# Kernel tuning notes

Hardware: AMD Instinct MI355X
Metric: run time of the kernel (lower is better)

Reference implementation:

```python
import jax, jax.numpy as jnp
import numpy as np

N_NODES = 50000
N_EDGES = 800000
IN_F = 128
HID = 64
HEADS = 4
N_CLASSES = 256
NEG_SLOPE = 0.2


def _gat_layer(h, W, al, ar, b, src, dst, act):
    """One DGL-style GATConv. h:[N,Din], W:[Din,H*F], al/ar:[H,F], b:[H*F].
    Returns [N,H,F]."""
    N = h.shape[0]
    H, F = al.shape
    z = (h @ W).reshape(N, H, F)                       # projected feats
    el = jnp.einsum('nhf,hf->nh', z, al)               # [N,H] src score part
    er = jnp.einsum('nhf,hf->nh', z, ar)               # [N,H] dst score part
    e = jax.nn.leaky_relu(el[src] + er[dst], negative_slope=NEG_SLOPE)  # [E,H]
    # segment softmax over incoming edges of each destination node
    emax = jax.ops.segment_max(e, dst, num_segments=N)                  # [N,H]
    ex = jnp.exp(e - emax[dst])                                         # [E,H]
    den = jax.ops.segment_sum(ex, dst, num_segments=N)                  # [N,H]
    alpha = ex / jnp.maximum(den[dst], 1e-9)                            # [E,H]
    msg = z[src] * alpha[:, :, None]                                    # [E,H,F]
    out = jax.ops.segment_sum(msg, dst, num_segments=N)                 # [N,H,F]
    out = out + b.reshape(1, H, F)
    return act(out) if act is not None else out


def setup_inputs() -> dict:
    key = jax.random.key(0)
    ks = jax.random.split(key, 16)
    feat = jax.random.normal(ks[0], (N_NODES, IN_F), dtype=jnp.float32)
    src = jax.random.randint(ks[1], (N_EDGES,), 0, N_NODES, dtype=jnp.int32)
    dst = jax.random.randint(ks[2], (N_EDGES,), 0, N_NODES, dtype=jnp.int32)

    def glorot(k, shape):
        fan = shape[0] + shape[-1]
        return jax.random.normal(k, shape, dtype=jnp.float32) * np.sqrt(2.0 / fan)

    # layer 0: IN_F -> HEADS*HID
    W0 = glorot(ks[3], (IN_F, HEADS * HID))
    al0 = glorot(ks[4], (HEADS, HID))
    ar0 = glorot(ks[5], (HEADS, HID))
    b0 = jnp.zeros((HEADS * HID,), dtype=jnp.float32)
    # layer 1: HEADS*HID -> HEADS*HID
    W1 = glorot(ks[6], (HEADS * HID, HEADS * HID))
    al1 = glorot(ks[7], (HEADS, HID))
    ar1 = glorot(ks[8], (HEADS, HID))
    b1 = jnp.zeros((HEADS * HID,), dtype=jnp.float32)
    # final layer: HEADS*HID -> HEADS*N_CLASSES
    W2 = glorot(ks[9], (HEADS * HID, HEADS * N_CLASSES))
    al2 = glorot(ks[10], (HEADS, N_CLASSES))
    ar2 = glorot(ks[11], (HEADS, N_CLASSES))
    b2 = jnp.zeros((HEADS * N_CLASSES,), dtype=jnp.float32)
    return {"feat": feat,
            "W0": W0, "al0": al0, "ar0": ar0, "b0": b0,
            "W1": W1, "al1": al1, "ar1": ar1, "b1": b1,
            "W2": W2, "al2": al2, "ar2": ar2, "b2": b2,
            "src": src, "dst": dst}


def reference(feat, W0, al0, ar0, b0, W1, al1, ar1, b1, W2, al2, ar2, b2, src, dst):
    elu = jax.nn.elu
    h = _gat_layer(feat, W0, al0, ar0, b0, src, dst, elu).reshape(N_NODES, -1)
    h = _gat_layer(h, W1, al1, ar1, b1, src, dst, elu).reshape(N_NODES, -1)
    logits = _gat_layer(h, W2, al2, ar2, b2, src, dst, None).mean(axis=1)  # [N, C]
    return logits
```

## Files before the change

kernel.cpp:

```cpp
#include <hip/hip_runtime.h>
#include <hip/hip_bf16.h>


#define NN 50000
#define NE 800000
#define NH_HEADS 4

typedef __attribute__((ext_vector_type(8))) short short8;
typedef __attribute__((ext_vector_type(8))) _Float16 half8;
typedef __attribute__((ext_vector_type(4))) _Float16 half4;
typedef __attribute__((ext_vector_type(4))) float floatx4;

__device__ inline float bf2f(short s) {
    union { unsigned u; float f; } v; v.u = ((unsigned)(unsigned short)s) << 16;
    return v.f;
}
__device__ inline short f2bf_rne(float x) {
    union { float f; unsigned u; } v; v.f = x;
    unsigned r = v.u + 0x7fff + ((v.u >> 16) & 1);
    return (short)(r >> 16);
}
__device__ inline void split1(float x, short& h, short& l) {
    union { float f; unsigned u; } v; v.f = x;
    h = (short)(v.u >> 16);
    union { float f; unsigned u; } rv; rv.f = v.f - bf2f(h);
    l = (short)(rv.u >> 16);
}

__device__ inline void load_lds16(const void* g, void* l) {
    __builtin_amdgcn_global_load_lds(
        (const __attribute__((address_space(1))) void*)g,
        (__attribute__((address_space(3))) void*)l, 16, 0, 0);
}


__global__ void hist_kernel(const int* __restrict__ dst, int* __restrict__ deg, int E) {
    int e = blockIdx.x * 256 + threadIdx.x;
    if (e < E) atomicAdd(&deg[dst[e]], 1);
}

__global__ void scan_block_kernel(const int* __restrict__ deg, int* __restrict__ offs,
                                  int* __restrict__ bsums, int n) {
    __shared__ int s[256];
    int tid = threadIdx.x;
    int i = blockIdx.x * 256 + tid;
    int v = (i < n) ? deg[i] : 0;
    s[tid] = v;
    __syncthreads();
    for (int off = 1; off < 256; off <<= 1) {
        int x = (tid >= off) ? s[tid - off] : 0;
        __syncthreads();
        s[tid] += x;
        __syncthreads();
    }
    if (i < n) offs[i] = s[tid] - v;
    if (tid == 255) bsums[blockIdx.x] = s[255];
}

__global__ void scan_sums_kernel(const int* __restrict__ bsums, int* __restrict__ boffs, int nb) {
    __shared__ int s[256];
    int tid = threadIdx.x;
    int v = (tid < nb) ? bsums[tid] : 0;
    s[tid] = v;
    __syncthreads();
    for (int off = 1; off < 256; off <<= 1) {
        int x = (tid >= off) ? s[tid - off] : 0;
        __syncthreads();
        s[tid] += x;
        __syncthreads();
    }
    boffs[tid] = s[tid] - v;
}

__global__ void add_offs_kernel(int* __restrict__ offs, const int* __restrict__ boffs,
                                int* __restrict__ cursor, int n, int total) {
    int i = blockIdx.x * 256 + threadIdx.x;
    if (i < n) {
        int o = offs[i] + boffs[blockIdx.x];
        offs[i] = o;
        cursor[i] = o;
    }
    if (i == 0) offs[n] = total;
}

__global__ void scatter_kernel(const int* __restrict__ src, const int* __restrict__ dst,
                               int* __restrict__ cursor, int* __restrict__ psrc, int E) {
    int e = blockIdx.x * 256 + threadIdx.x;
    if (e < E) {
        int p = atomicAdd(&cursor[dst[e]], 1);
        psrc[p] = src[e];
    }
}


__global__ __launch_bounds__(256) void splitA_rm(const float* __restrict__ A,
                                                 short* __restrict__ hi,
                                                 short* __restrict__ lo,
                                                 int total8) {
    int tid = blockIdx.x * 256 + threadIdx.x;
    if (tid >= total8) return;
    const float* p = A + (size_t)tid * 8;
    float4 x0 = ((const float4*)p)[0];
    float4 x1 = ((const float4*)p)[1];
    float xs[8] = {x0.x, x0.y, x0.z, x0.w, x1.x, x1.y, x1.z, x1.w};
    short8 hv, lv;
#pragma unroll
    for (int j = 0; j < 8; ++j) { short h, l; split1(xs[j], h, l); hv[j] = h; lv[j] = l; }
    ((short8*)hi)[tid] = hv;
    ((short8*)lo)[tid] = lv;
}


__global__ __launch_bounds__(256) void splitB_kernel(const float* __restrict__ B,
                                                     short* __restrict__ hi,
                                                     short* __restrict__ lo,
                                                     int K, int N) {
    int tid = blockIdx.x * 256 + threadIdx.x;
    int NG = N >> 4;
    int total = (K >> 5) * NG * 64;
    if (tid >= total) return;
    int lane = tid & 63;
    int rc = tid >> 6;
    int g = rc % NG, c = rc / NG;
    int n = g * 16 + (lane & 15);
    int k = c * 32 + (lane >> 4) * 8;
    short8 hv, lv;
#pragma unroll
    for (int j = 0; j < 8; ++j) {
        float x = B[(size_t)(k + j) * N + n];
        short h = f2bf_rne(x);
        hv[j] = h;
        lv[j] = f2bf_rne(x - bf2f(h));
    }
    ((short8*)hi)[tid] = hv;
    ((short8*)lo)[tid] = lv;
}

__global__ __launch_bounds__(256) void splitB_f16_kernel(const float* __restrict__ B,
                                                         _Float16* __restrict__ hi,
                                                         _Float16* __restrict__ lo,
                                                         int K, int N) {
    int tid = blockIdx.x * 256 + threadIdx.x;
    int NG = N >> 4;
    int total = (K >> 5) * NG * 64;
    if (tid >= total) return;
    int lane = tid & 63;
    int rc = tid >> 6;
    int g = rc % NG, c = rc / NG;
    int n = g * 16 + (lane & 15);
    int k = c * 32 + (lane >> 4) * 8;
    half8 hv, lv;
#pragma unroll
    for (int j = 0; j < 8; ++j) {
        float x = B[(size_t)(k + j) * N + n];
        _Float16 h = (_Float16)x;
        hv[j] = h;
        lv[j] = (_Float16)(x - (float)h);
    }
    ((half8*)hi)[tid] = hv;
    ((half8*)lo)[tid] = lv;
}

__global__ __launch_bounds__(256) void splitB2_f16s_kernel(const float* __restrict__ W2,
                                                           _Float16* __restrict__ hi) {
    int tid = blockIdx.x * 256 + threadIdx.x;
    const int NG = 16;
    int total = (1024 >> 5) * NG * 64;
    if (tid >= total) return;
    int lane = tid & 63;
    int rc = tid >> 6;
    int g = rc % NG, c = rc / NG;
    int n = g * 16 + (lane & 15);
    int kk = c * 32 + (lane >> 4) * 8;
    half8 hv;
#pragma unroll
    for (int j = 0; j < 8; ++j) {
        int kg = kk + j;
        int h = kg >> 8, k = kg & 255;
        hv[j] = (_Float16)W2[(size_t)k * 1024 + h * 256 + n];
    }
    ((half8*)hi)[tid] = hv;
}


__device__ inline floatx4 mfma16(short8 a, short8 b, floatx4 c) {
    return __builtin_amdgcn_mfma_f32_16x16x32_bf16(a, b, c, 0, 0, 0);
}
__device__ inline floatx4 mfma16h(half8 a, half8 b, floatx4 c) {
    return __builtin_amdgcn_mfma_f32_16x16x32_f16(a, b, c, 0, 0, 0);
}

__global__ __launch_bounds__(256) void gemm_n256l(const short* __restrict__ Ahi,
                                                  const short* __restrict__ Alo,
                                                  const short* __restrict__ Bh,
                                                  const short* __restrict__ Bl,
                                                  _Float16* __restrict__ Cf,
                                                  const float* __restrict__ alv,
                                                  const float* __restrict__ arv,
                                                  float* __restrict__ elo,
                                                  float* __restrict__ ero,
                                                  int M, int K) {
    int KC = K >> 5;
    __shared__ short AhL[2048];
    __shared__ short AlL[2048];
    int t = threadIdx.x;
    int lane = t & 63;
    int w = t >> 6;
    int bm = blockIdx.x * 64;
    int g0 = w * 4;
    const short8* pBh = (const short8*)Bh;
    const short8* pBl = (const short8*)Bl;

    floatx4 acc[4][4] = {};

    int row = bm + (w << 4) + (lane & 15);
    if (row >= M) row = M - 1;
    const short* gh = Ahi + (size_t)row * K + ((lane >> 4) << 3);
    const short* gl = Alo + (size_t)row * K + ((lane >> 4) << 3);
    short* lh = AhL + w * 512;
    short* ll = AlL + w * 512;

    for (int c = 0; c < KC; ++c) {
        load_lds16(gh + (size_t)c * 32, lh);
        load_lds16(gl + (size_t)c * 32, ll);
        short8 bh[4], bl[4];
#pragma unroll
        for (int g = 0; g < 4; ++g) {
            bh[g] = pBh[((size_t)c * 16 + g0 + g) * 64 + lane];
            bl[g] = pBl[((size_t)c * 16 + g0 + g) * 64 + lane];
        }
        __syncthreads();
#pragma unroll
        for (int mt = 0; mt < 4; ++mt) {
            short8 ah = *(const short8*)(AhL + mt * 512 + lane * 8);
            short8 al = *(const short8*)(AlL + mt * 512 + lane * 8);
#pragma unroll
            for (int g = 0; g < 4; ++g) {
                acc[mt][g] = mfma16(ah, bh[g], acc[mt][g]);
                acc[mt][g] = mfma16(al, bh[g], acc[mt][g]);
                acc[mt][g] = mfma16(ah, bl[g], acc[mt][g]);
            }
        }
        __syncthreads();
    }

    int rowb = bm + (lane >> 4) * 4;
    int colb = w * 64 + (lane & 15);
#pragma unroll
    for (int mt = 0; mt < 4; ++mt) {
#pragma unroll
        for (int r = 0; r < 4; ++r) {
            int rr = rowb + mt * 16 + r;
            if (rr < M) {
#pragma unroll
                for (int g = 0; g < 4; ++g) {
                    Cf[(size_t)rr * 256 + colb + g * 16] = (_Float16)acc[mt][g][r];
                }
            }
        }
    }

    if (alv) {
        float alr[4], arr_[4];
#pragma unroll
        for (int g = 0; g < 4; ++g) {
            int f = w * 64 + (lane & 15) + g * 16;
            alr[g] = alv[f];
            arr_[g] = arv[f];
        }
#pragma unroll
        for (int mt = 0; mt < 4; ++mt) {
#pragma unroll
            for (int r = 0; r < 4; ++r) {
                float se = acc[mt][0][r] * alr[0] + acc[mt][1][r] * alr[1] +
                           acc[mt][2][r] * alr[2] + acc[mt][3][r] * alr[3];
                float sr = acc[mt][0][r] * arr_[0] + acc[mt][1][r] * arr_[1] +
                           acc[mt][2][r] * arr_[2] + acc[mt][3][r] * arr_[3];
                se += __shfl_xor(se, 1); se += __shfl_xor(se, 2);
                se += __shfl_xor(se, 4); se += __shfl_xor(se, 8);
                sr += __shfl_xor(sr, 1); sr += __shfl_xor(sr, 2);
                sr += __shfl_xor(sr, 4); sr += __shfl_xor(sr, 8);
                int rr = rowb + mt * 16 + r;
                if ((lane & 15) == 0 && rr < M) {
                    elo[rr * 4 + w] = se;
                    ero[rr * 4 + w] = sr;
                }
            }
        }
    }
}

__global__ __launch_bounds__(256) void gemm_f16_n256(const _Float16* __restrict__ A,
                                                     const _Float16* __restrict__ Bh,
                                                     const _Float16* __restrict__ Bl,
                                                     _Float16* __restrict__ Cf,
                                                     const float* __restrict__ alv,
                                                     const float* __restrict__ arv,
                                                     float* __restrict__ elo,
                                                     float* __restrict__ ero,
                                                     int M, int K) {
    int KC = K >> 5;
    __shared__ _Float16 AL[2048];
    int t = threadIdx.x;
    int lane = t & 63;
    int w = t >> 6;
    int bm = blockIdx.x * 64;
    int g0 = w * 4;
    const half8* pBh = (const half8*)Bh;
    const half8* pBl = (const half8*)Bl;

    floatx4 acc[4][4] = {};

    int row = bm + (w << 4) + (lane & 15);
    if (row >= M) row = M - 1;
    const _Float16* gA = A + (size_t)row * K + ((lane >> 4) << 3);
    _Float16* lA = AL + w * 512;

    for (int c = 0; c < KC; ++c) {
        load_lds16(gA + (size_t)c * 32, lA);
        half8 bh[4], bl[4];
#pragma unroll
        for (int g = 0; g < 4; ++g) {
            bh[g] = pBh[((size_t)c * 16 + g0 + g) * 64 + lane];
            bl[g] = pBl[((size_t)c * 16 + g0 + g) * 64 + lane];
        }
        __syncthreads();
#pragma unroll
        for (int mt = 0; mt < 4; ++mt) {
            half8 a = *(const half8*)(AL + mt * 512 + lane * 8);
#pragma unroll
            for (int g = 0; g < 4; ++g) {
                acc[mt][g] = mfma16h(a, bh[g], acc[mt][g]);
                acc[mt][g] = mfma16h(a, bl[g], acc[mt][g]);
            }
        }
        __syncthreads();
    }

    int rowb = bm + (lane >> 4) * 4;
    int colb = w * 64 + (lane & 15);
#pragma unroll
    for (int mt = 0; mt < 4; ++mt) {
#pragma unroll
        for (int r = 0; r < 4; ++r) {
            int rr = rowb + mt * 16 + r;
            if (rr < M) {
#pragma unroll
                for (int g = 0; g < 4; ++g) {
                    Cf[(size_t)rr * 256 + colb + g * 16] = (_Float16)acc[mt][g][r];
                }
            }
        }
    }

    if (alv) {
        float alr[4], arr_[4];
#pragma unroll
        for (int g = 0; g < 4; ++g) {
            int f = w * 64 + (lane & 15) + g * 16;
            alr[g] = alv[f];
            arr_[g] = arv[f];
        }
#pragma unroll
        for (int mt = 0; mt < 4; ++mt) {
#pragma unroll
            for (int r = 0; r < 4; ++r) {
                float se = acc[mt][0][r] * alr[0] + acc[mt][1][r] * alr[1] +
                           acc[mt][2][r] * alr[2] + acc[mt][3][r] * alr[3];
                float sr = acc[mt][0][r] * arr_[0] + acc[mt][1][r] * arr_[1] +
                           acc[mt][2][r] * arr_[2] + acc[mt][3][r] * arr_[3];
                se += __shfl_xor(se, 1); se += __shfl_xor(se, 2);
                se += __shfl_xor(se, 4); se += __shfl_xor(se, 8);
                sr += __shfl_xor(sr, 1); sr += __shfl_xor(sr, 2);
                sr += __shfl_xor(sr, 4); sr += __shfl_xor(sr, 8);
                int rr = rowb + mt * 16 + r;
                if ((lane & 15) == 0 && rr < M) {
                    elo[rr * 4 + w] = se;
                    ero[rr * 4 + w] = sr;
                }
            }
        }
    }
}

__global__ __launch_bounds__(256) void gemm_f16_ns2(const _Float16* __restrict__ A,
                                                    const _Float16* __restrict__ Bh,
                                                    const float* __restrict__ bias4,
                                                    float* __restrict__ C,
                                                    int M, int K) {
    int KC = K >> 5;
    __shared__ _Float16 AL[2048];
    int t = threadIdx.x;
    int lane = t & 63;
    int w = t >> 6;
    int bm = blockIdx.x * 64;
    int g0 = blockIdx.y * 8 + w * 2;
    const half8* pBh = (const half8*)Bh;

    floatx4 acc[4][2] = {};

    int row = bm + (w << 4) + (lane & 15);
    if (row >= M) row = M - 1;
    const _Float16* gA = A + (size_t)row * K + ((lane >> 4) << 3);
    _Float16* lA = AL + w * 512;

    for (int c = 0; c < KC; ++c) {
        load_lds16(gA + (size_t)c * 32, lA);
        half8 bh[2];
#pragma unroll
        for (int g = 0; g < 2; ++g) {
            bh[g] = pBh[((size_t)c * 16 + g0 + g) * 64 + lane];
        }
        __syncthreads();
#pragma unroll
        for (int mt = 0; mt < 4; ++mt) {
            half8 a = *(const half8*)(AL + mt * 512 + lane * 8);
#pragma unroll
            for (int g = 0; g < 2; ++g) {
                acc[mt][g] = mfma16h(a, bh[g], acc[mt][g]);
            }
        }
        __syncthreads();
    }

    int rowb = bm + (lane >> 4) * 4;
    int colb = blockIdx.y * 128 + w * 32 + (lane & 15);
#pragma unroll
    for (int mt = 0; mt < 4; ++mt) {
#pragma unroll
        for (int r = 0; r < 4; ++r) {
            int rr = rowb + mt * 16 + r;
            if (rr < M) {
#pragma unroll
                for (int g = 0; g < 2; ++g) {
                    int col = colb + g * 16;
                    float v = acc[mt][g][r];
                    v = 0.25f * (v + bias4[col] + bias4[col + 256] +
                                 bias4[col + 512] + bias4[col + 768]);
                    C[(size_t)rr * 256 + col] = v;
                }
            }
        }
    }
}


__global__ __launch_bounds__(256) void proj_av_kernel(const float* __restrict__ W2,
                                                      const float* __restrict__ al2,
                                                      const float* __restrict__ ar2,
                                                      float* __restrict__ val,
                                                      float* __restrict__ var_) {
    int gid = blockIdx.x * 256 + threadIdx.x;
    int w = gid >> 6;
    int lane = threadIdx.x & 63;
    if (w >= 1024) return;
    int h = w >> 8, k = w & 255;
    const float* wrow = W2 + (size_t)k * 1024 + h * 256;
    const float* ap = al2 + h * 256;
    const float* rp = ar2 + h * 256;
    float sv = 0.f, sr = 0.f;
    for (int j = lane; j < 256; j += 64) {
        float x = wrow[j];
        sv += x * ap[j];
        sr += x * rp[j];
    }
#pragma unroll
    for (int off = 32; off > 0; off >>= 1) {
        sv += __shfl_down(sv, off);
        sr += __shfl_down(sr, off);
    }
    if (lane == 0) { val[w] = sv; var_[w] = sr; }
}

__global__ __launch_bounds__(256) void elr2_kernel(const _Float16* __restrict__ h1,
                                                   const float* __restrict__ val,
                                                   const float* __restrict__ var_,
                                                   float* __restrict__ el,
                                                   float* __restrict__ er) {
    int gid = blockIdx.x * 256 + threadIdx.x;
    int w = gid >> 6;
    int lane = threadIdx.x & 63;
    if (w >= NN * 4) return;
    int n = w >> 2, h = w & 3;
    const _Float16* hr = h1 + (size_t)n * 256;
    const float* vp = val + h * 256;
    const float* rp = var_ + h * 256;
    float se = 0.f, sr = 0.f;
    for (int k = lane; k < 256; k += 64) {
        float x = (float)hr[k];
        se += x * vp[k];
        sr += x * rp[k];
    }
#pragma unroll
    for (int off = 32; off > 0; off >>= 1) {
        se += __shfl_down(se, off);
        sr += __shfl_down(sr, off);
    }
    if (lane == 0) { el[w] = se; er[w] = sr; }
}


__global__ __launch_bounds__(64) void agg_z64_kernel(const _Float16* __restrict__ z,
                                                     const float* __restrict__ el,
                                                     const float* __restrict__ er,
                                                     const int* __restrict__ offs,
                                                     const int* __restrict__ psrc,
                                                     const float* __restrict__ bias,
                                                     _Float16* __restrict__ out) {
    int n = blockIdx.x;
    int l = threadIdx.x;
    __shared__ float p_lds[16][4];
    __shared__ int src_lds[16];
    __shared__ float den_lds[4];
    if (l < 4) den_lds[l] = 0.f;
    int e_local = l >> 2, hh = l & 3;
    int h = l >> 4;
    float er_n = er[n * 4 + hh];
    int beg = offs[n], end = offs[n + 1];
    float a0 = 0.f, a1 = 0.f, a2 = 0.f, a3 = 0.f;
    for (int base = beg; base < end; base += 16) {
        int cnt = min(16, end - base);
        __syncthreads();
        float p = 0.f;
        if (e_local < cnt) {
            int s = psrc[base + e_local];
            if (hh == 0) src_lds[e_local] = s;
            float sc = el[s * 4 + hh] + er_n;
            sc = (sc > 0.f) ? sc : 0.2f * sc;
            p = __expf(sc);
            p_lds[e_local][hh] = p;
        }
        float d = p;
        d += __shfl_xor(d, 4);  d += __shfl_xor(d, 8);
        d += __shfl_xor(d, 16); d += __shfl_xor(d, 32);
        if (l < 4) den_lds[l] += d;
        __syncthreads();
        for (int e = 0; e < cnt; ++e) {
            half4 v = *(const half4*)(z + (size_t)src_lds[e] * 256 + (l << 2));
            float pe = p_lds[e][h];
            a0 += pe * (float)v[0];
            a1 += pe * (float)v[1];
            a2 += pe * (float)v[2];
            a3 += pe * (float)v[3];
        }
    }
    __syncthreads();
    float rd = 1.f / fmaxf(den_lds[h], 1e-9f);
    float vals[4] = {a0, a1, a2, a3};
    half4 o;
#pragma unroll
    for (int j = 0; j < 4; ++j) {
        float x = vals[j] * rd + bias[(l << 2) + j];
        x = (x > 0.f) ? x : (__expf(x) - 1.f);
        o[j] = (_Float16)x;
    }
    *(half4*)(out + (size_t)n * 256 + (l << 2)) = o;
}

__global__ __launch_bounds__(64) void aggH_64_kernel(const _Float16* __restrict__ h1,
                                                     const float* __restrict__ el,
                                                     const float* __restrict__ er,
                                                     const int* __restrict__ offs,
                                                     const int* __restrict__ psrc,
                                                     _Float16* __restrict__ oA) {
    int n = blockIdx.x;
    int l = threadIdx.x;
    __shared__ __align__(16) float p_lds[16][4];
    __shared__ int src_lds[16];
    __shared__ float den_lds[4];
    if (l < 4) den_lds[l] = 0.f;
    int e_local = l >> 2, hh = l & 3;
    float er_n = er[n * 4 + hh];
    int beg = offs[n], end = offs[n + 1];
    float acc[4][4] = {};
    for (int base = beg; base < end; base += 16) {
        int cnt = min(16, end - base);
        __syncthreads();
        float p = 0.f;
        if (e_local < cnt) {
            int s = psrc[base + e_local];
            if (hh == 0) src_lds[e_local] = s;
            float sc = el[s * 4 + hh] + er_n;
            sc = (sc > 0.f) ? sc : 0.2f * sc;
            p = __expf(sc);
            p_lds[e_local][hh] = p;
        }
        float d = p;
        d += __shfl_xor(d, 4);  d += __shfl_xor(d, 8);
        d += __shfl_xor(d, 16); d += __shfl_xor(d, 32);
        if (l < 4) den_lds[l] += d;
        __syncthreads();
        for (int e = 0; e < cnt; ++e) {
            half4 v = *(const half4*)(h1 + (size_t)src_lds[e] * 256 + (l << 2));
            float vf0 = (float)v[0], vf1 = (float)v[1];
            float vf2 = (float)v[2], vf3 = (float)v[3];
            floatx4 pv = *(const floatx4*)&p_lds[e][0];
#pragma unroll
            for (int hd = 0; hd < 4; ++hd) {
                acc[hd][0] += pv[hd] * vf0;
                acc[hd][1] += pv[hd] * vf1;
                acc[hd][2] += pv[hd] * vf2;
                acc[hd][3] += pv[hd] * vf3;
            }
        }
    }
    __syncthreads();
    size_t base_o = (size_t)n * 1024 + (l << 2);
#pragma unroll
    for (int hd = 0; hd < 4; ++hd) {
        float rd = 1.f / fmaxf(den_lds[hd], 1e-9f);
        half4 o;
#pragma unroll
        for (int j = 0; j < 4; ++j) o[j] = (_Float16)(acc[hd][j] * rd);
        *(half4*)(oA + base_o + hd * 256) = o;
    }
}


extern "C" void kernel_launch(void* const* d_in, const int* in_sizes, int n_in,
                              void* d_out, int out_size, void* d_ws, size_t ws_size,
                              hipStream_t stream) {
    const float* feat = (const float*)d_in[0];
    const float* W0 = (const float*)d_in[1];
    const float* al0 = (const float*)d_in[2];
    const float* ar0 = (const float*)d_in[3];
    const float* b0 = (const float*)d_in[4];
    const float* W1 = (const float*)d_in[5];
    const float* al1 = (const float*)d_in[6];
    const float* ar1 = (const float*)d_in[7];
    const float* b1 = (const float*)d_in[8];
    const float* W2 = (const float*)d_in[9];
    const float* al2 = (const float*)d_in[10];
    const float* ar2 = (const float*)d_in[11];
    const float* b2 = (const float*)d_in[12];
    const int* src = (const int*)d_in[13];
    const int* dst = (const int*)d_in[14];
    float* out = (float*)d_out;

    float* slotA = (float*)d_ws;
    _Float16* zh = (_Float16*)slotA;
    short* feathi = (short*)(slotA + (size_t)NN * 256);
    short* featlo = feathi + (size_t)NN * 128;
    _Float16* Af16 = (_Float16*)slotA;
    float* slotB = slotA + (size_t)NN * 1024;
    _Float16* h0f = (_Float16*)slotB;
    _Float16* h1h = (_Float16*)slotB;
    float* el = slotB + (size_t)NN * 256;
    float* er = el + (size_t)NN * NH_HEADS;
    int* deg = (int*)(er + (size_t)NN * NH_HEADS);
    int* offs = deg + NN;
    int* cursor = offs + NN + 2;
    int* bsums = cursor + NN;
    int* boffs = bsums + 256;
    int* psrc = boffs + 256;
    short* Bh = (short*)(psrc + NE + 2);
    short* Bl = Bh + 262144;
    float* val = (float*)(Bl + 262144);
    float* var_ = val + 1024;

    hipMemsetAsync(deg, 0, NN * sizeof(int), stream);
    hist_kernel<<<(NE + 255) / 256, 256, 0, stream>>>(dst, deg, NE);
    int nb = (NN + 255) / 256;
    scan_block_kernel<<<nb, 256, 0, stream>>>(deg, offs, bsums, NN);
    scan_sums_kernel<<<1, 256, 0, stream>>>(bsums, boffs, nb);
    add_offs_kernel<<<nb, 256, 0, stream>>>(offs, boffs, cursor, NN, NE);
    scatter_kernel<<<(NE + 255) / 256, 256, 0, stream>>>(src, dst, cursor, psrc, NE);

    int mb64 = (NN + 63) / 64;

    splitA_rm<<<(NN * 128 / 8 + 255) / 256, 256, 0, stream>>>(feat, feathi, featlo, NN * 128 / 8);
    splitB_kernel<<<(4096 + 255) / 256, 256, 0, stream>>>(W0, Bh, Bl, 128, 256);
    gemm_n256l<<<mb64, 256, 0, stream>>>(feathi, featlo, Bh, Bl, zh,
                                         al0, ar0, el, er, NN, 128);
    agg_z64_kernel<<<NN, 64, 0, stream>>>(zh, el, er, offs, psrc, b0, h0f);

    splitB_f16_kernel<<<(8192 + 255) / 256, 256, 0, stream>>>(W1, (_Float16*)Bh,
                                                              (_Float16*)Bl, 256, 256);
    gemm_f16_n256<<<mb64, 256, 0, stream>>>(h0f, (const _Float16*)Bh, (const _Float16*)Bl,
                                            zh, al1, ar1, el, er, NN, 256);
    agg_z64_kernel<<<NN, 64, 0, stream>>>(zh, el, er, offs, psrc, b1, h1h);

    proj_av_kernel<<<256, 256, 0, stream>>>(W2, al2, ar2, val, var_);
    elr2_kernel<<<NN, 256, 0, stream>>>(h1h, val, var_, el, er);
    aggH_64_kernel<<<NN, 64, 0, stream>>>(h1h, el, er, offs, psrc, Af16);
    splitB2_f16s_kernel<<<(32768 + 255) / 256, 256, 0, stream>>>(W2, (_Float16*)Bh);
    dim3 gfin(mb64, 2);
    gemm_f16_ns2<<<gfin, 256, 0, stream>>>(Af16, (const _Float16*)Bh, b2, out, NN, 1024);
}
```

Baseline: 571.5 us.

## Split layer-0/1 GEMMs across two column blocks and accumulate attention scores atomically

The two N=256 projection GEMMs now launch a 2D grid, so each block computes 128 output columns instead of 256. This doubles the block count and halves the per-thread accumulator registers. Each head's el/er dot product is now split across two waves, so partial sums are combined with atomicAdd into buffers zeroed by new memsets. The cost is that A tiles are loaded twice, plus the extra memsets and atomic traffic. The memset assumes el and er are contiguous (NN*8 floats).

```diff
diff --git a/kernel.cpp b/kernel.cpp
--- a/kernel.cpp
+++ b/kernel.cpp
@@ -207,11 +207,11 @@
     int lane = t & 63;
     int w = t >> 6;
     int bm = blockIdx.x * 64;
-    int g0 = w * 4;
+    int g0 = blockIdx.y * 8 + w * 2;
     const short8* pBh = (const short8*)Bh;
     const short8* pBl = (const short8*)Bl;
 
-    floatx4 acc[4][4] = {};
+    floatx4 acc[4][2] = {};
 
     int row = bm + (w << 4) + (lane & 15);
     if (row >= M) row = M - 1;
@@ -223,9 +223,9 @@
     for (int c = 0; c < KC; ++c) {
         load_lds16(gh + (size_t)c * 32, lh);
         load_lds16(gl + (size_t)c * 32, ll);
-        short8 bh[4], bl[4];
-#pragma unroll
-        for (int g = 0; g < 4; ++g) {
+        short8 bh[2], bl[2];
+#pragma unroll
+        for (int g = 0; g < 2; ++g) {
             bh[g] = pBh[((size_t)c * 16 + g0 + g) * 64 + lane];
             bl[g] = pBl[((size_t)c * 16 + g0 + g) * 64 + lane];
         }
@@ -235,7 +235,7 @@
             short8 ah = *(const short8*)(AhL + mt * 512 + lane * 8);
             short8 al = *(const short8*)(AlL + mt * 512 + lane * 8);
 #pragma unroll
-            for (int g = 0; g < 4; ++g) {
+            for (int g = 0; g < 2; ++g) {
                 acc[mt][g] = mfma16(ah, bh[g], acc[mt][g]);
                 acc[mt][g] = mfma16(al, bh[g], acc[mt][g]);
                 acc[mt][g] = mfma16(ah, bl[g], acc[mt][g]);
@@ -245,7 +245,7 @@
     }
 
     int rowb = bm + (lane >> 4) * 4;
-    int colb = w * 64 + (lane & 15);
+    int colb = blockIdx.y * 128 + w * 32 + (lane & 15);
 #pragma unroll
     for (int mt = 0; mt < 4; ++mt) {
 #pragma unroll
@@ -253,7 +253,7 @@
             int rr = rowb + mt * 16 + r;
             if (rr < M) {
 #pragma unroll
-                for (int g = 0; g < 4; ++g) {
+                for (int g = 0; g < 2; ++g) {
                     Cf[(size_t)rr * 256 + colb + g * 16] = (_Float16)acc[mt][g][r];
                 }
             }
@@ -261,29 +261,27 @@
     }
 
     if (alv) {
-        float alr[4], arr_[4];
-#pragma unroll
-        for (int g = 0; g < 4; ++g) {
-            int f = w * 64 + (lane & 15) + g * 16;
-            alr[g] = alv[f];
-            arr_[g] = arv[f];
+        int head = blockIdx.y * 2 + (w >> 1);
+        float alr[2], arr_[2];
+#pragma unroll
+        for (int g = 0; g < 2; ++g) {
+            alr[g] = alv[colb + g * 16];
+            arr_[g] = arv[colb + g * 16];
         }
 #pragma unroll
         for (int mt = 0; mt < 4; ++mt) {
 #pragma unroll
             for (int r = 0; r < 4; ++r) {
-                float se = acc[mt][0][r] * alr[0] + acc[mt][1][r] * alr[1] +
-                           acc[mt][2][r] * alr[2] + acc[mt][3][r] * alr[3];
-                float sr = acc[mt][0][r] * arr_[0] + acc[mt][1][r] * arr_[1] +
-                           acc[mt][2][r] * arr_[2] + acc[mt][3][r] * arr_[3];
+                float se = acc[mt][0][r] * alr[0] + acc[mt][1][r] * alr[1];
+                float sr = acc[mt][0][r] * arr_[0] + acc[mt][1][r] * arr_[1];
                 se += __shfl_xor(se, 1); se += __shfl_xor(se, 2);
                 se += __shfl_xor(se, 4); se += __shfl_xor(se, 8);
                 sr += __shfl_xor(sr, 1); sr += __shfl_xor(sr, 2);
                 sr += __shfl_xor(sr, 4); sr += __shfl_xor(sr, 8);
                 int rr = rowb + mt * 16 + r;
                 if ((lane & 15) == 0 && rr < M) {
-                    elo[rr * 4 + w] = se;
-                    ero[rr * 4 + w] = sr;
+                    atomicAdd(&elo[rr * 4 + head], se);
+                    atomicAdd(&ero[rr * 4 + head], sr);
                 }
             }
         }
@@ -305,11 +303,11 @@
     int lane = t & 63;
     int w = t >> 6;
     int bm = blockIdx.x * 64;
-    int g0 = w * 4;
+    int g0 = blockIdx.y * 8 + w * 2;
     const half8* pBh = (const half8*)Bh;
     const half8* pBl = (const half8*)Bl;
 
-    floatx4 acc[4][4] = {};
+    floatx4 acc[4][2] = {};
 
     int row = bm + (w << 4) + (lane & 15);
     if (row >= M) row = M - 1;
@@ -318,9 +316,9 @@
 
     for (int c = 0; c < KC; ++c) {
         load_lds16(gA + (size_t)c * 32, lA);
-        half8 bh[4], bl[4];
-#pragma unroll
-        for (int g = 0; g < 4; ++g) {
+        half8 bh[2], bl[2];
+#pragma unroll
+        for (int g = 0; g < 2; ++g) {
             bh[g] = pBh[((size_t)c * 16 + g0 + g) * 64 + lane];
             bl[g] = pBl[((size_t)c * 16 + g0 + g) * 64 + lane];
         }
@@ -329,7 +327,7 @@
         for (int mt = 0; mt < 4; ++mt) {
             half8 a = *(const half8*)(AL + mt * 512 + lane * 8);
 #pragma unroll
-            for (int g = 0; g < 4; ++g) {
+            for (int g = 0; g < 2; ++g) {
                 acc[mt][g] = mfma16h(a, bh[g], acc[mt][g]);
                 acc[mt][g] = mfma16h(a, bl[g], acc[mt][g]);
             }
@@ -338,7 +336,7 @@
     }
 
     int rowb = bm + (lane >> 4) * 4;
-    int colb = w * 64 + (lane & 15);
+    int colb = blockIdx.y * 128 + w * 32 + (lane & 15);
 #pragma unroll
     for (int mt = 0; mt < 4; ++mt) {
 #pragma unroll
@@ -346,7 +344,7 @@
             int rr = rowb + mt * 16 + r;
             if (rr < M) {
 #pragma unroll
-                for (int g = 0; g < 4; ++g) {
+                for (int g = 0; g < 2; ++g) {
                     Cf[(size_t)rr * 256 + colb + g * 16] = (_Float16)acc[mt][g][r];
                 }
             }
@@ -354,29 +352,27 @@
     }
 
     if (alv) {
-        float alr[4], arr_[4];
-#pragma unroll
-        for (int g = 0; g < 4; ++g) {
-            int f = w * 64 + (lane & 15) + g * 16;
-            alr[g] = alv[f];
-            arr_[g] = arv[f];
+        int head = blockIdx.y * 2 + (w >> 1);
+        float alr[2], arr_[2];
+#pragma unroll
+        for (int g = 0; g < 2; ++g) {
+            alr[g] = alv[colb + g * 16];
+            arr_[g] = arv[colb + g * 16];
         }
 #pragma unroll
         for (int mt = 0; mt < 4; ++mt) {
 #pragma unroll
             for (int r = 0; r < 4; ++r) {
-                float se = acc[mt][0][r] * alr[0] + acc[mt][1][r] * alr[1] +
-                           acc[mt][2][r] * alr[2] + acc[mt][3][r] * alr[3];
-                float sr = acc[mt][0][r] * arr_[0] + acc[mt][1][r] * arr_[1] +
-                           acc[mt][2][r] * arr_[2] + acc[mt][3][r] * arr_[3];
+                float se = acc[mt][0][r] * alr[0] + acc[mt][1][r] * alr[1];
+                float sr = acc[mt][0][r] * arr_[0] + acc[mt][1][r] * arr_[1];
                 se += __shfl_xor(se, 1); se += __shfl_xor(se, 2);
                 se += __shfl_xor(se, 4); se += __shfl_xor(se, 8);
                 sr += __shfl_xor(sr, 1); sr += __shfl_xor(sr, 2);
                 sr += __shfl_xor(sr, 4); sr += __shfl_xor(sr, 8);
                 int rr = rowb + mt * 16 + r;
                 if ((lane & 15) == 0 && rr < M) {
-                    elo[rr * 4 + w] = se;
-                    ero[rr * 4 + w] = sr;
+                    atomicAdd(&elo[rr * 4 + head], se);
+                    atomicAdd(&ero[rr * 4 + head], sr);
                 }
             }
         }
@@ -667,23 +663,25 @@
     scatter_kernel<<<(NE + 255) / 256, 256, 0, stream>>>(src, dst, cursor, psrc, NE);
 
     int mb64 = (NN + 63) / 64;
+    dim3 g2(mb64, 2);
 
     splitA_rm<<<(NN * 128 / 8 + 255) / 256, 256, 0, stream>>>(feat, feathi, featlo, NN * 128 / 8);
     splitB_kernel<<<(4096 + 255) / 256, 256, 0, stream>>>(W0, Bh, Bl, 128, 256);
-    gemm_n256l<<<mb64, 256, 0, stream>>>(feathi, featlo, Bh, Bl, zh,
-                                         al0, ar0, el, er, NN, 128);
+    hipMemsetAsync(el, 0, (size_t)NN * 8 * sizeof(float), stream);
+    gemm_n256l<<<g2, 256, 0, stream>>>(feathi, featlo, Bh, Bl, zh,
+                                       al0, ar0, el, er, NN, 128);
     agg_z64_kernel<<<NN, 64, 0, stream>>>(zh, el, er, offs, psrc, b0, h0f);
 
     splitB_f16_kernel<<<(8192 + 255) / 256, 256, 0, stream>>>(W1, (_Float16*)Bh,
                                                               (_Float16*)Bl, 256, 256);
-    gemm_f16_n256<<<mb64, 256, 0, stream>>>(h0f, (const _Float16*)Bh, (const _Float16*)Bl,
-                                            zh, al1, ar1, el, er, NN, 256);
+    hipMemsetAsync(el, 0, (size_t)NN * 8 * sizeof(float), stream);
+    gemm_f16_n256<<<g2, 256, 0, stream>>>(h0f, (const _Float16*)Bh, (const _Float16*)Bl,
+                                          zh, al1, ar1, el, er, NN, 256);
     agg_z64_kernel<<<NN, 64, 0, stream>>>(zh, el, er, offs, psrc, b1, h1h);
 
     proj_av_kernel<<<256, 256, 0, stream>>>(W2, al2, ar2, val, var_);
     elr2_kernel<<<NN, 256, 0, stream>>>(h1h, val, var_, el, er);
     aggH_64_kernel<<<NN, 64, 0, stream>>>(h1h, el, er, offs, psrc, Af16);
     splitB2_f16s_kernel<<<(32768 + 255) / 256, 256, 0, stream>>>(W2, (_Float16*)Bh);
-    dim3 gfin(mb64, 2);
-    gemm_f16_ns2<<<gfin, 256, 0, stream>>>(Af16, (const _Float16*)Bh, b2, out, NN, 1024);
-}
+    gemm_f16_ns2<<<g2, 256, 0, stream>>>(Af16, (const _Float16*)Bh, b2, out, NN, 1024);
+}
```

After: 638.7 us. 11.8% more time.
